# Optimization experiments

Hardware: AMD Instinct MI355X
Metric: run time of the kernel (lower is better)

## Reference

```python
import jax, jax.numpy as jnp
import numpy as np
import math

B, S, D, H = 4, 2048, 1024, 16
DK = D // H

def setup_inputs() -> dict:
    key = jax.random.key(0)
    ks = jax.random.split(key, 8)
    scale = 1.0 / math.sqrt(D)
    q = jax.random.normal(ks[0], (B, S, D), dtype=jnp.float32)
    k = jax.random.normal(ks[1], (B, S, D), dtype=jnp.float32)
    v = jax.random.normal(ks[2], (B, S, D), dtype=jnp.float32)
    Wq = jax.random.normal(ks[3], (D, D), dtype=jnp.float32) * scale
    Wk = jax.random.normal(ks[4], (D, D), dtype=jnp.float32) * scale
    Wv = jax.random.normal(ks[5], (D, D), dtype=jnp.float32) * scale
    Wo = jax.random.normal(ks[6], (D, D), dtype=jnp.float32) * scale
    # causal mask, broadcast over batch and heads (masked_fill where mask == 0)
    mask = jnp.tril(jnp.ones((S, S), dtype=jnp.int32))[None, None, :, :]
    return {"q": q, "k": k, "v": v, "Wq": Wq, "Wk": Wk, "Wv": Wv, "Wo": Wo, "mask": mask}

def reference(q, k, v, Wq, Wk, Wv, Wo, mask):
    # Linear projections (nn.Linear: x @ W^T), split heads -> [B, H, S, DK]
    def split_heads(x, W):
        y = jnp.einsum('bsd,ed->bse', x, W)
        return y.reshape(x.shape[0], x.shape[1], H, DK).transpose(0, 2, 1, 3)
    qh = split_heads(q, Wq)
    kh = split_heads(k, Wk)
    vh = split_heads(v, Wv)
    scores = jnp.einsum('bhqd,bhkd->bhqk', qh, kh) / math.sqrt(DK)  # [B,H,S,S]
    scores = jnp.where(mask == 0, -jnp.inf, scores)
    p = jax.nn.softmax(scores, axis=-1)
    ctx = jnp.einsum('bhqk,bhkd->bhqd', p, vh)
    ctx = ctx.transpose(0, 2, 1, 3).reshape(q.shape[0], q.shape[1], H * DK)
    return jnp.einsum('bsd,ed->bse', ctx, Wo)
```

## Files before the change

kernel.cpp:

```cpp
#include <hip/hip_runtime.h>

#define BB 4
#define SS 2048
#define DD 1024
#define HH 16
#define DKK 64
#define MTOT (BB * SS)
#define QKV_N (MTOT * DD)
#define W_N (DD * DD)

typedef __attribute__((ext_vector_type(8))) short short8;
typedef __attribute__((ext_vector_type(4))) float f32x4;
typedef __attribute__((ext_vector_type(4))) unsigned short u16x4;
typedef unsigned short ushort_t;

#define GP(p) ((__attribute__((address_space(1))) void*)(p))
#define LP(p) ((__attribute__((address_space(3))) void*)(p))

__device__ __forceinline__ ushort_t f2bf(float f) {
    union { float f; unsigned u; } c; c.f = f;
    unsigned r = c.u + 0x7fffu + ((c.u >> 16) & 1u);
    return (ushort_t)(r >> 16);
}

__global__ __launch_bounds__(256)
void cvt2(const float* __restrict__ s0, ushort_t* __restrict__ d0, int n0,
          const float* __restrict__ s1, ushort_t* __restrict__ d1, int n1)
{
    int i = (blockIdx.x * 256 + threadIdx.x) * 4;
    const float* s; ushort_t* d; int off;
    if (i < n0) { s = s0; d = d0; off = i; }
    else        { s = s1; d = d1; off = i - n0; if (off >= n1) return; }
    f32x4 x = *(const f32x4*)(s + off);
    u16x4 h;
    h[0] = f2bf(x[0]); h[1] = f2bf(x[1]); h[2] = f2bf(x[2]); h[3] = f2bf(x[3]);
    *(u16x4*)(d + off) = h;
}

template<int MODE>
__global__ __launch_bounds__(256, 2)
void gemm_m97(const ushort_t* __restrict__ A, const ushort_t* __restrict__ W,
              void* __restrict__ out, float scale)
{
    __shared__ ushort_t As[128 * 32];
    __shared__ ushort_t Bs[128 * 32];

    const int tid  = threadIdx.x;
    const int lane = tid & 63;
    const int w    = tid >> 6;
    const int wm   = w >> 1, wn = w & 1;
    const int l15  = lane & 15, l4 = lane >> 4;
    const int m0   = blockIdx.x * 128;
    const int n0   = blockIdx.y * 128;

    f32x4 acc[4][4] = {};

    for (int kk = 0; kk < 1024; kk += 32) {
        #pragma unroll
        for (int i = 0; i < 2; ++i) {
            int c  = i * 256 + w * 64 + lane;
            int r  = c >> 2;
            int cb = (c & 3) ^ (r & 3);
            __builtin_amdgcn_global_load_lds(
                GP(A + (size_t)(m0 + r) * 1024 + kk + cb * 8), LP(As + c * 8), 16, 0, 0);
            __builtin_amdgcn_global_load_lds(
                GP(W + (size_t)(n0 + r) * 1024 + kk + cb * 8), LP(Bs + c * 8), 16, 0, 0);
        }
        __syncthreads();

        short8 af[4], bfr[4];
        #pragma unroll
        for (int mi = 0; mi < 4; ++mi) {
            int row = wm * 64 + mi * 16 + l15;
            af[mi] = *(const short8*)(As + (row * 4 + (l4 ^ (row & 3))) * 8);
        }
        #pragma unroll
        for (int ni = 0; ni < 4; ++ni) {
            int row = wn * 64 + ni * 16 + l15;
            bfr[ni] = *(const short8*)(Bs + (row * 4 + (l4 ^ (row & 3))) * 8);
        }
        #pragma unroll
        for (int mi = 0; mi < 4; ++mi)
            #pragma unroll
            for (int ni = 0; ni < 4; ++ni)
                acc[mi][ni] = __builtin_amdgcn_mfma_f32_16x16x32_bf16(
                    af[mi], bfr[ni], acc[mi][ni], 0, 0, 0);
        __syncthreads();
    }

    #pragma unroll
    for (int mi = 0; mi < 4; ++mi) {
        int rowb = m0 + wm * 64 + mi * 16 + l4 * 4;
        #pragma unroll
        for (int ni = 0; ni < 4; ++ni) {
            int n = n0 + wn * 64 + ni * 16 + l15;
            if constexpr (MODE == 0) {
                int h = n >> 6, dk = n & 63;
                #pragma unroll
                for (int r = 0; r < 4; ++r) {
                    int m = rowb + r, b = m >> 11, s = m & 2047;
                    ((ushort_t*)out)[(((size_t)(b * 16 + h) * 2048 + s) << 6) + dk] =
                        f2bf(acc[mi][ni][r] * scale);
                }
            } else if constexpr (MODE == 1) {
                int h = n >> 6, dk = n & 63;
                int b = rowb >> 11, s0v = rowb & 2047;
                u16x4 hh;
                #pragma unroll
                for (int r = 0; r < 4; ++r) hh[r] = f2bf(acc[mi][ni][r]);
                *(u16x4*)((ushort_t*)out + (((size_t)(b * 16 + h) << 6) + dk) * 2048 + s0v) = hh;
            } else {
                #pragma unroll
                for (int r = 0; r < 4; ++r)
                    ((float*)out)[(size_t)(rowb + r) * 1024 + n] = acc[mi][ni][r];
            }
        }
    }
}

__global__ __launch_bounds__(256, 2)
void attn_fwd2(const ushort_t* __restrict__ Qh, const ushort_t* __restrict__ Kh,
               const ushort_t* __restrict__ Vt, ushort_t* __restrict__ Ctx)
{
    __shared__ ushort_t Kl[64 * 64];
    __shared__ ushort_t Vl[64 * 64];
    __shared__ ushort_t Pl[4][32][72];

    const int tid  = threadIdx.x;
    const int lane = tid & 63;
    const int w    = tid >> 6;
    const int l15  = lane & 15, l4 = lane >> 4;
    const int idx  = blockIdx.x;
    const int qt   = 15 - (idx >> 6);
    const int bh   = idx & 63;
    const int b    = bh >> 4, h = bh & 15;
    const int q0   = qt * 128;
    const ushort_t* Qb = Qh + (size_t)bh * SS * DKK;
    const ushort_t* Kb = Kh + (size_t)bh * SS * DKK;
    const ushort_t* Vb = Vt + (size_t)bh * DKK * SS;

    short8 qf[2][2];
    #pragma unroll
    for (int mi = 0; mi < 2; ++mi)
        #pragma unroll
        for (int ks = 0; ks < 2; ++ks) {
            int row = q0 + w * 32 + mi * 16 + l15;
            qf[mi][ks] = *(const short8*)(Qb + (size_t)row * 64 + ks * 32 + l4 * 8);
        }

    float m_i[2][4], l_i[2][4];
    f32x4 O[2][4] = {};
    #pragma unroll
    for (int mi = 0; mi < 2; ++mi)
        #pragma unroll
        for (int r = 0; r < 4; ++r) { m_i[mi][r] = -__builtin_inff(); l_i[mi][r] = 0.f; }

    const int nkt = 2 * qt + 2;
    for (int kt = 0; kt < nkt; ++kt) {
        const int k0 = kt * 64;
        #pragma unroll
        for (int i = 0; i < 2; ++i) {
            int c  = i * 256 + w * 64 + lane;
            int r  = c >> 3;
            int cb = (c & 7) ^ (r & 7);
            __builtin_amdgcn_global_load_lds(
                GP(Kb + (size_t)(k0 + r) * 64 + cb * 8), LP(Kl + c * 8), 16, 0, 0);
            __builtin_amdgcn_global_load_lds(
                GP(Vb + (size_t)r * 2048 + k0 + cb * 8), LP(Vl + c * 8), 16, 0, 0);
        }
        __syncthreads();

        short8 kf[4][2];
        #pragma unroll
        for (int ni = 0; ni < 4; ++ni)
            #pragma unroll
            for (int ks = 0; ks < 2; ++ks) {
                int r = ni * 16 + l15, cb = ks * 4 + l4;
                kf[ni][ks] = *(const short8*)(Kl + (r * 8 + (cb ^ (r & 7))) * 8);
            }

        f32x4 sc[2][4] = {};
        #pragma unroll
        for (int mi = 0; mi < 2; ++mi)
            #pragma unroll
            for (int ni = 0; ni < 4; ++ni)
                #pragma unroll
                for (int ks = 0; ks < 2; ++ks)
                    sc[mi][ni] = __builtin_amdgcn_mfma_f32_16x16x32_bf16(
                        qf[mi][ks], kf[ni][ks], sc[mi][ni], 0, 0, 0);

        #pragma unroll
        for (int mi = 0; mi < 2; ++mi)
            #pragma unroll
            for (int ni = 0; ni < 4; ++ni)
                #pragma unroll
                for (int r = 0; r < 4; ++r) {
                    int kcol = k0 + ni * 16 + l15;
                    int qrow = q0 + w * 32 + mi * 16 + l4 * 4 + r;
                    if (kcol > qrow) sc[mi][ni][r] = -__builtin_inff();
                }

        #pragma unroll
        for (int mi = 0; mi < 2; ++mi)
            #pragma unroll
            for (int r = 0; r < 4; ++r) {
                float mx = sc[mi][0][r];
                #pragma unroll
                for (int ni = 1; ni < 4; ++ni) mx = fmaxf(mx, sc[mi][ni][r]);
                #pragma unroll
                for (int d = 1; d < 16; d <<= 1) mx = fmaxf(mx, __shfl_xor(mx, d, 64));
                float mnew  = fmaxf(m_i[mi][r], mx);
                float alpha = __expf(m_i[mi][r] - mnew);
                float rs = 0.f;
                #pragma unroll
                for (int ni = 0; ni < 4; ++ni) {
                    float p = __expf(sc[mi][ni][r] - mnew);
                    sc[mi][ni][r] = p;
                    rs += p;
                }
                #pragma unroll
                for (int d = 1; d < 16; d <<= 1) rs += __shfl_xor(rs, d, 64);
                l_i[mi][r] = l_i[mi][r] * alpha + rs;
                m_i[mi][r] = mnew;
                #pragma unroll
                for (int nd = 0; nd < 4; ++nd) O[mi][nd][r] *= alpha;
            }

        #pragma unroll
        for (int mi = 0; mi < 2; ++mi)
            #pragma unroll
            for (int ni = 0; ni < 4; ++ni)
                #pragma unroll
                for (int r = 0; r < 4; ++r)
                    Pl[w][mi * 16 + l4 * 4 + r][ni * 16 + l15] = f2bf(sc[mi][ni][r]);

        short8 pf[2][2], vf[2][4];
        #pragma unroll
        for (int mi = 0; mi < 2; ++mi)
            #pragma unroll
            for (int ks = 0; ks < 2; ++ks)
                pf[mi][ks] = *(const short8*)(&Pl[w][mi * 16 + l15][ks * 32 + l4 * 8]);
        #pragma unroll
        for (int ks = 0; ks < 2; ++ks)
            #pragma unroll
            for (int nd = 0; nd < 4; ++nd) {
                int r = nd * 16 + l15, cb = ks * 4 + l4;
                vf[ks][nd] = *(const short8*)(Vl + (r * 8 + (cb ^ (r & 7))) * 8);
            }

        #pragma unroll
        for (int mi = 0; mi < 2; ++mi)
            #pragma unroll
            for (int nd = 0; nd < 4; ++nd)
                #pragma unroll
                for (int ks = 0; ks < 2; ++ks)
                    O[mi][nd] = __builtin_amdgcn_mfma_f32_16x16x32_bf16(
                        pf[mi][ks], vf[ks][nd], O[mi][nd], 0, 0, 0);

        __syncthreads();
    }

    #pragma unroll
    for (int mi = 0; mi < 2; ++mi)
        #pragma unroll
        for (int nd = 0; nd < 4; ++nd)
            #pragma unroll
            for (int r = 0; r < 4; ++r) {
                int row = q0 + w * 32 + mi * 16 + l4 * 4 + r;
                int dk  = nd * 16 + l15;
                float o = O[mi][nd][r] / l_i[mi][r];
                Ctx[((size_t)b * 2048 + row) * 1024 + h * 64 + dk] = f2bf(o);
            }
}

extern "C" void kernel_launch(void* const* d_in, const int* in_sizes, int n_in,
                              void* d_out, int out_size, void* d_ws, size_t ws_size,
                              hipStream_t stream)
{
    const float* q  = (const float*)d_in[0];
    const float* k  = (const float*)d_in[1];
    const float* v  = (const float*)d_in[2];
    const float* Wq = (const float*)d_in[3];
    const float* Wk = (const float*)d_in[4];
    const float* Wv = (const float*)d_in[5];
    const float* Wo = (const float*)d_in[6];
    float* out = (float*)d_out;

    ushort_t* B0 = (ushort_t*)d_ws;
    ushort_t* B1 = B0 + (size_t)QKV_N;
    ushort_t* B2 = B1 + (size_t)QKV_N;
    ushort_t* B3 = B2 + (size_t)QKV_N;
    ushort_t* wbE = (ushort_t*)d_out;
    dim3 gg(MTOT / 128, DD / 128);
    const int cvtg = (QKV_N + W_N) / 1024;

    cvt2<<<cvtg, 256, 0, stream>>>(q, B0, QKV_N, Wq, wbE, W_N);
    gemm_m97<0><<<gg, 256, 0, stream>>>(B0, wbE, B1, 0.125f);

    cvt2<<<cvtg, 256, 0, stream>>>(k, B0, QKV_N, Wk, wbE, W_N);
    gemm_m97<0><<<gg, 256, 0, stream>>>(B0, wbE, B2, 1.0f);

    cvt2<<<cvtg, 256, 0, stream>>>(v, B0, QKV_N, Wv, wbE, W_N);
    gemm_m97<1><<<gg, 256, 0, stream>>>(B0, wbE, B3, 1.0f);

    attn_fwd2<<<1024, 256, 0, stream>>>(B1, B2, B3, B0);

    cvt2<<<W_N / 1024, 256, 0, stream>>>(Wo, B1, W_N, Wo, B1, 0);
    gemm_m97<2><<<gg, 256, 0, stream>>>(B0, B1, out, 1.0f);
}
```

Baseline: 389.5 us.

## Restructure attention loop with K/V prefetch, transposed scores, exp2 softmax

Reworks the attention kernel to compute S^T (K as A operand) so each lane owns one query row, which cuts the cross-lane max and sum reductions to two shuffles. The softmax scale is folded into the Q projection as log2(e)/8 so the kernel can use exp2. K/V tiles are read into registers and the next tile is then issued to LDS asynchronously so the copy overlaps compute. Waves whose rows sit entirely above the diagonal skip the tile, masking only runs on diagonal tiles, and occupancy is raised to 3 blocks. P and output stores become vectorized; the risk is more register pressure and a second barrier per iteration.

After: 442.3 us. +13.6%, slower.

```diff
diff --git a/kernel.cpp b/kernel.cpp
--- a/kernel.cpp
+++ b/kernel.cpp
@@ -16,6 +16,13 @@
 
 #define GP(p) ((__attribute__((address_space(1))) void*)(p))
 #define LP(p) ((__attribute__((address_space(3))) void*)(p))
+
+#if __has_builtin(__builtin_amdgcn_exp2f)
+#define EXP2(x) __builtin_amdgcn_exp2f(x)
+#else
+#define EXP2(x) __expf((x) * 0.6931471805599453f)
+#endif
+#define QSCALE 0.1803368801111204f
 
 __device__ __forceinline__ ushort_t f2bf(float f) {
     union { float f; unsigned u; } c; c.f = f;
@@ -118,8 +125,8 @@
     }
 }
 
-__global__ __launch_bounds__(256, 2)
-void attn_fwd2(const ushort_t* __restrict__ Qh, const ushort_t* __restrict__ Kh,
+__global__ __launch_bounds__(256, 3)
+void attn_fwd4(const ushort_t* __restrict__ Qh, const ushort_t* __restrict__ Kh,
                const ushort_t* __restrict__ Vt, ushort_t* __restrict__ Ctx)
 {
     __shared__ ushort_t Kl[64 * 64];
@@ -141,23 +148,19 @@
 
     short8 qf[2][2];
     #pragma unroll
-    for (int mi = 0; mi < 2; ++mi)
+    for (int qg = 0; qg < 2; ++qg)
         #pragma unroll
         for (int ks = 0; ks < 2; ++ks) {
-            int row = q0 + w * 32 + mi * 16 + l15;
-            qf[mi][ks] = *(const short8*)(Qb + (size_t)row * 64 + ks * 32 + l4 * 8);
-        }
-
-    float m_i[2][4], l_i[2][4];
-    f32x4 O[2][4] = {};
-    #pragma unroll
-    for (int mi = 0; mi < 2; ++mi)
-        #pragma unroll
-        for (int r = 0; r < 4; ++r) { m_i[mi][r] = -__builtin_inff(); l_i[mi][r] = 0.f; }
-
-    const int nkt = 2 * qt + 2;
-    for (int kt = 0; kt < nkt; ++kt) {
-        const int k0 = kt * 64;
+            int row = q0 + w * 32 + qg * 16 + l15;
+            qf[qg][ks] = *(const short8*)(Qb + (size_t)row * 64 + ks * 32 + l4 * 8);
+        }
+
+    f32x4 Ot[2][4] = {};
+    float m_i[2], l_i[2];
+    m_i[0] = m_i[1] = -__builtin_inff();
+    l_i[0] = l_i[1] = 0.f;
+
+    auto stage = [&](int k0) {
         #pragma unroll
         for (int i = 0; i < 2; ++i) {
             int c  = i * 256 + w * 64 + lane;
@@ -168,109 +171,134 @@
             __builtin_amdgcn_global_load_lds(
                 GP(Vb + (size_t)r * 2048 + k0 + cb * 8), LP(Vl + c * 8), 16, 0, 0);
         }
+    };
+
+    const int nkt = 2 * qt + 2;
+    const int wrow0 = q0 + w * 32;
+    stage(0);
+
+    for (int kt = 0; kt < nkt; ++kt) {
+        const int k0 = kt * 64;
+        const bool act = (k0 <= wrow0 + 31);
         __syncthreads();
 
-        short8 kf[4][2];
-        #pragma unroll
-        for (int ni = 0; ni < 4; ++ni)
-            #pragma unroll
-            for (int ks = 0; ks < 2; ++ks) {
-                int r = ni * 16 + l15, cb = ks * 4 + l4;
-                kf[ni][ks] = *(const short8*)(Kl + (r * 8 + (cb ^ (r & 7))) * 8);
+        short8 kf[4][2], vf[2][4];
+        if (act) {
+            #pragma unroll
+            for (int ni = 0; ni < 4; ++ni)
+                #pragma unroll
+                for (int ks = 0; ks < 2; ++ks) {
+                    int r = ni * 16 + l15, cb = ks * 4 + l4;
+                    kf[ni][ks] = *(const short8*)(Kl + (r * 8 + (cb ^ (r & 7))) * 8);
+                }
+            #pragma unroll
+            for (int ks = 0; ks < 2; ++ks)
+                #pragma unroll
+                for (int nd = 0; nd < 4; ++nd) {
+                    int r = nd * 16 + l15, cb = ks * 4 + l4;
+                    vf[ks][nd] = *(const short8*)(Vl + (r * 8 + (cb ^ (r & 7))) * 8);
+                }
+        }
+        __syncthreads();
+        if (kt + 1 < nkt) stage(k0 + 64);
+        if (!act) continue;
+
+        f32x4 sc[2][4] = {};
+        #pragma unroll
+        for (int qg = 0; qg < 2; ++qg)
+            #pragma unroll
+            for (int ni = 0; ni < 4; ++ni)
+                #pragma unroll
+                for (int ks = 0; ks < 2; ++ks)
+                    sc[qg][ni] = __builtin_amdgcn_mfma_f32_16x16x32_bf16(
+                        kf[ni][ks], qf[qg][ks], sc[qg][ni], 0, 0, 0);
+
+        if (k0 + 63 > wrow0) {
+            #pragma unroll
+            for (int qg = 0; qg < 2; ++qg) {
+                int qrow = wrow0 + qg * 16 + l15;
+                #pragma unroll
+                for (int ni = 0; ni < 4; ++ni)
+                    #pragma unroll
+                    for (int r = 0; r < 4; ++r) {
+                        int kcol = k0 + ni * 16 + l4 * 4 + r;
+                        if (kcol > qrow) sc[qg][ni][r] = -1.0e30f;
+                    }
             }
-
-        f32x4 sc[2][4] = {};
-        #pragma unroll
-        for (int mi = 0; mi < 2; ++mi)
-            #pragma unroll
-            for (int ni = 0; ni < 4; ++ni)
-                #pragma unroll
-                for (int ks = 0; ks < 2; ++ks)
-                    sc[mi][ni] = __builtin_amdgcn_mfma_f32_16x16x32_bf16(
-                        qf[mi][ks], kf[ni][ks], sc[mi][ni], 0, 0, 0);
-
-        #pragma unroll
-        for (int mi = 0; mi < 2; ++mi)
+        }
+
+        #pragma unroll
+        for (int qg = 0; qg < 2; ++qg) {
+            float mx = sc[qg][0][0];
+            #pragma unroll
+            for (int ni = 0; ni < 4; ++ni)
+                #pragma unroll
+                for (int r = 0; r < 4; ++r) mx = fmaxf(mx, sc[qg][ni][r]);
+            mx = fmaxf(mx, __shfl_xor(mx, 16, 64));
+            mx = fmaxf(mx, __shfl_xor(mx, 32, 64));
+            float mnew  = fmaxf(m_i[qg], mx);
+            float alpha = EXP2(m_i[qg] - mnew);
+            float rs = 0.f;
             #pragma unroll
             for (int ni = 0; ni < 4; ++ni)
                 #pragma unroll
                 for (int r = 0; r < 4; ++r) {
-                    int kcol = k0 + ni * 16 + l15;
-                    int qrow = q0 + w * 32 + mi * 16 + l4 * 4 + r;
-                    if (kcol > qrow) sc[mi][ni][r] = -__builtin_inff();
-                }
-
-        #pragma unroll
-        for (int mi = 0; mi < 2; ++mi)
-            #pragma unroll
-            for (int r = 0; r < 4; ++r) {
-                float mx = sc[mi][0][r];
-                #pragma unroll
-                for (int ni = 1; ni < 4; ++ni) mx = fmaxf(mx, sc[mi][ni][r]);
-                #pragma unroll
-                for (int d = 1; d < 16; d <<= 1) mx = fmaxf(mx, __shfl_xor(mx, d, 64));
-                float mnew  = fmaxf(m_i[mi][r], mx);
-                float alpha = __expf(m_i[mi][r] - mnew);
-                float rs = 0.f;
-                #pragma unroll
-                for (int ni = 0; ni < 4; ++ni) {
-                    float p = __expf(sc[mi][ni][r] - mnew);
-                    sc[mi][ni][r] = p;
+                    float p = EXP2(sc[qg][ni][r] - mnew);
+                    sc[qg][ni][r] = p;
                     rs += p;
                 }
-                #pragma unroll
-                for (int d = 1; d < 16; d <<= 1) rs += __shfl_xor(rs, d, 64);
-                l_i[mi][r] = l_i[mi][r] * alpha + rs;
-                m_i[mi][r] = mnew;
-                #pragma unroll
-                for (int nd = 0; nd < 4; ++nd) O[mi][nd][r] *= alpha;
+            rs += __shfl_xor(rs, 16, 64);
+            rs += __shfl_xor(rs, 32, 64);
+            l_i[qg] = l_i[qg] * alpha + rs;
+            m_i[qg] = mnew;
+            #pragma unroll
+            for (int nd = 0; nd < 4; ++nd)
+                #pragma unroll
+                for (int r = 0; r < 4; ++r) Ot[qg][nd][r] *= alpha;
+        }
+
+        #pragma unroll
+        for (int qg = 0; qg < 2; ++qg) {
+            int qr = qg * 16 + l15;
+            #pragma unroll
+            for (int ni = 0; ni < 4; ++ni) {
+                u16x4 hh;
+                #pragma unroll
+                for (int r = 0; r < 4; ++r) hh[r] = f2bf(sc[qg][ni][r]);
+                *(u16x4*)(&Pl[w][qr][ni * 16 + l4 * 4]) = hh;
             }
-
-        #pragma unroll
-        for (int mi = 0; mi < 2; ++mi)
-            #pragma unroll
-            for (int ni = 0; ni < 4; ++ni)
-                #pragma unroll
-                for (int r = 0; r < 4; ++r)
-                    Pl[w][mi * 16 + l4 * 4 + r][ni * 16 + l15] = f2bf(sc[mi][ni][r]);
-
-        short8 pf[2][2], vf[2][4];
-        #pragma unroll
-        for (int mi = 0; mi < 2; ++mi)
+        }
+
+        short8 pT[2][2];
+        #pragma unroll
+        for (int qg = 0; qg < 2; ++qg)
             #pragma unroll
             for (int ks = 0; ks < 2; ++ks)
-                pf[mi][ks] = *(const short8*)(&Pl[w][mi * 16 + l15][ks * 32 + l4 * 8]);
-        #pragma unroll
-        for (int ks = 0; ks < 2; ++ks)
-            #pragma unroll
-            for (int nd = 0; nd < 4; ++nd) {
-                int r = nd * 16 + l15, cb = ks * 4 + l4;
-                vf[ks][nd] = *(const short8*)(Vl + (r * 8 + (cb ^ (r & 7))) * 8);
-            }
-
-        #pragma unroll
-        for (int mi = 0; mi < 2; ++mi)
+                pT[qg][ks] = *(const short8*)(&Pl[w][qg * 16 + l15][ks * 32 + l4 * 8]);
+
+        #pragma unroll
+        for (int qg = 0; qg < 2; ++qg)
             #pragma unroll
             for (int nd = 0; nd < 4; ++nd)
                 #pragma unroll
                 for (int ks = 0; ks < 2; ++ks)
-                    O[mi][nd] = __builtin_amdgcn_mfma_f32_16x16x32_bf16(
-                        pf[mi][ks], vf[ks][nd], O[mi][nd], 0, 0, 0);
-
-        __syncthreads();
+                    Ot[qg][nd] = __builtin_amdgcn_mfma_f32_16x16x32_bf16(
+                        vf[ks][nd], pT[qg][ks], Ot[qg][nd], 0, 0, 0);
     }
 
     #pragma unroll
-    for (int mi = 0; mi < 2; ++mi)
-        #pragma unroll
-        for (int nd = 0; nd < 4; ++nd)
-            #pragma unroll
-            for (int r = 0; r < 4; ++r) {
-                int row = q0 + w * 32 + mi * 16 + l4 * 4 + r;
-                int dk  = nd * 16 + l15;
-                float o = O[mi][nd][r] / l_i[mi][r];
-                Ctx[((size_t)b * 2048 + row) * 1024 + h * 64 + dk] = f2bf(o);
-            }
+    for (int qg = 0; qg < 2; ++qg) {
+        float inv = 1.0f / l_i[qg];
+        int qrow = q0 + w * 32 + qg * 16 + l15;
+        ushort_t* dst = Ctx + ((size_t)b * 2048 + qrow) * 1024 + h * 64;
+        #pragma unroll
+        for (int nd = 0; nd < 4; ++nd) {
+            u16x4 hh;
+            #pragma unroll
+            for (int r = 0; r < 4; ++r) hh[r] = f2bf(Ot[qg][nd][r] * inv);
+            *(u16x4*)(dst + nd * 16 + l4 * 4) = hh;
+        }
+    }
 }
 
 extern "C" void kernel_launch(void* const* d_in, const int* in_sizes, int n_in,
@@ -295,7 +323,7 @@
     const int cvtg = (QKV_N + W_N) / 1024;
 
     cvt2<<<cvtg, 256, 0, stream>>>(q, B0, QKV_N, Wq, wbE, W_N);
-    gemm_m97<0><<<gg, 256, 0, stream>>>(B0, wbE, B1, 0.125f);
+    gemm_m97<0><<<gg, 256, 0, stream>>>(B0, wbE, B1, QSCALE);
 
     cvt2<<<cvtg, 256, 0, stream>>>(k, B0, QKV_N, Wk, wbE, W_N);
     gemm_m97<0><<<gg, 256, 0, stream>>>(B0, wbE, B2, 1.0f);
@@ -303,7 +331,7 @@
     cvt2<<<cvtg, 256, 0, stream>>>(v, B0, QKV_N, Wv, wbE, W_N);
     gemm_m97<1><<<gg, 256, 0, stream>>>(B0, wbE, B3, 1.0f);
 
-    attn_fwd2<<<1024, 256, 0, stream>>>(B1, B2, B3, B0);
+    attn_fwd4<<<1024, 256, 0, stream>>>(B1, B2, B3, B0);
 
     cvt2<<<W_N / 1024, 256, 0, stream>>>(Wo, B1, W_N, Wo, B1, 0);
     gemm_m97<2><<<gg, 256, 0, stream>>>(B0, B1, out, 1.0f);
```
